# Performance work log

Measured on AMD Instinct MI355X. Metric: run time of the kernel, lower is better.

The kernel has to match this reference:

```python
import jax, jax.numpy as jnp
from jax import lax
import numpy as np

LOGZERO = -1e10  # matches the repo's `logzero` sentinel


def setup_inputs() -> dict:
    key = jax.random.key(0)
    k1, k2, k3, k4 = jax.random.split(key, 4)
    bs, xmax, vocab, ymax = 32, 1024, 1000, 128
    # CTC log-probabilities (ctc_generator output is log_softmax in the repo)
    ctc_out = jax.nn.log_softmax(
        jax.random.normal(k1, (bs, xmax, vocab), jnp.float32), axis=-1)
    src_size = jax.random.randint(k2, (bs,), xmax // 2, xmax + 1)
    src_mask = (jnp.arange(xmax)[None, :] < src_size[:, None])[:, None, :]  # [bs,1,xmax] bool
    ys = jax.random.randint(k3, (bs, ymax), 1, vocab)   # non-blank labels
    ylens = jax.random.randint(k4, (bs,), ymax // 2, ymax + 1)
    return {"ctc_out": ctc_out, "src_mask": src_mask, "src_size": src_size,
            "ys": ys, "ylens": ylens, "blank": 0}


def reference(ctc_out, src_mask, src_size, ys, ylens, blank):
    bs, xmax, vocab = ctc_out.shape
    ymax = ys.shape[1]
    L = 2 * ymax + 1  # blank-interleaved path length

    # mask invalid frames to logzero (masked_fill in torch)
    lp = jnp.where(src_mask.transpose(0, 2, 1), ctc_out, LOGZERO)  # [bs,xmax,vocab]

    # blank-interleaved path: [blank, y1, blank, y2, ..., blank]
    path = jnp.full((bs, L), blank, dtype=ys.dtype).at[:, 1::2].set(ys)
    path_lens = 2 * ylens + 1

    # log-probs gathered along the path: [xmax, bs, L] (time-major for scan)
    lp_path = jnp.take_along_axis(
        lp, jnp.broadcast_to(path[:, None, :], (bs, xmax, L)), axis=2)
    lp_path = lp_path.transpose(1, 0, 2)

    same_tr = path[:, :-2] == path[:, 2:]                 # [bs, L-2]
    idx = jnp.arange(L)
    outside = idx[None, :] >= path_lens[:, None]          # [bs, L]

    alpha0 = jnp.full((bs, L), LOGZERO, jnp.float32).at[:, 0].set(0.0)

    def step(alpha, lp_t):
        m0 = alpha
        m1 = jnp.concatenate([jnp.full((bs, 1), LOGZERO, alpha.dtype), alpha[:, :-1]], axis=1)
        m2 = jnp.concatenate([jnp.full((bs, 2), LOGZERO, alpha.dtype),
                              jnp.where(same_tr, LOGZERO, alpha[:, :-2])], axis=1)
        mat = jnp.stack([m0, m1, m2])                     # [3, bs, L]
        max_prob = jnp.max(mat, axis=0)
        arg = jnp.argmax(mat, axis=0)
        bp_t = idx[None, :] - arg                          # back-pointer (path position)
        max_prob = jnp.where(outside, LOGZERO, max_prob)
        alpha_new = max_prob + lp_t
        return alpha_new, (alpha_new, bp_t)

    _, (alpha_hist, bp) = lax.scan(step, alpha0, lp_path)  # [xmax,bs,L] each
    alpha_full = jnp.concatenate([alpha0[None], alpha_hist], axis=0)  # [xmax+1,bs,L]

    b_idx = jnp.arange(bs)
    alpha_at = alpha_full[src_size, b_idx]                 # [bs, L] alpha at t = src_size
    s1 = alpha_at[b_idx, path_lens - 1]
    s2 = alpha_at[b_idx, path_lens - 2]
    start = jnp.where(s1 > s2, path_lens - 1, path_lens - 2)
    score = jnp.maximum(s1, s2)                            # best alignment log-prob per utt

    # vectorized backtrace over all batches (reverse scan over time)
    def back_step(carry, t):
        tt = jnp.minimum(t + 1, xmax - 1)
        prev = bp[tt, b_idx, carry]                        # bp[b, t+1, state_{t+1}]
        val = jnp.where(t == src_size - 1, start,
                        jnp.where(t < src_size - 1, prev, 0))
        return val, val

    ts = jnp.arange(xmax - 1, -1, -1)
    _, states_rev = lax.scan(back_step, jnp.zeros((bs,), start.dtype), ts)
    states = states_rev[::-1].T                            # [bs, xmax] path positions

    aligned = jnp.take_along_axis(path, states, axis=1)    # [bs, xmax] tokens
    shift = jnp.concatenate([jnp.zeros((bs, 1), aligned.dtype), aligned[:, :-1]], axis=1)
    aligned = jnp.where(aligned == shift, 0, aligned)      # collapse repeats to 0
    shift2 = jnp.concatenate([jnp.zeros((bs, 1), aligned.dtype), aligned[:, :-1]], axis=1)

    csum = jnp.cumsum((shift2 != blank).astype(jnp.int32), axis=1)  # [bs, xmax]
    tm = csum[:, None, :] == jnp.arange(ymax + 1)[None, :, None]    # [bs, ymax+1, xmax]
    last = tm[:, -1, :] & src_mask[:, 0, :]
    last = last.at[b_idx, src_size - 1].set(True)
    tm = tm.at[:, -1, :].set(last)
    trigger_mask = tm & src_mask                           # & x_mask from FaNat.forward

    return score, trigger_mask, ylens + 1
```

## Files before the change

### kernel.cpp

```cpp
#include <hip/hip_runtime.h>
#include <stdint.h>

#define LOGZERO (-1e10f)

static constexpr int BS    = 32;
static constexpr int XMAX  = 1024;
static constexpr int VOCAB = 1000;
static constexpr int YMAX  = 128;
static constexpr int NROWS = YMAX + 1;
static constexpr int CH    = 8;
static constexpr int NPROD = 8;
static constexpr int NWAVES = 1 + NPROD;
static constexpr int NPAIR = XMAX / 2;

__global__ __launch_bounds__(64 * NWAVES) void k_viterbi(
    const float* __restrict__ ctc, const int* __restrict__ src_size,
    const int* __restrict__ ys, const int* __restrict__ ylens,
    const int* __restrict__ blankp, int* __restrict__ csum_ws,
    float* __restrict__ out)
{
    __shared__ float buf[2][CH][256];
    __shared__ unsigned char  bpb[XMAX * 64];
    __shared__ unsigned char  bp256[XMAX];
    __shared__ unsigned short bp2[NPAIR * 64];
    __shared__ unsigned char  bp2_256[NPAIR];
    __shared__ unsigned short st_lds[XMAX];
    __shared__ int ysl[YMAX];

    const int b    = blockIdx.x;
    const int tid  = threadIdx.x;
    const int wid  = tid >> 6;
    const int lane = tid & 63;
    const int ss   = src_size[b];
    const int yl   = ylens[b];
    const int bv   = blankp[0];
    const int plen = 2 * yl + 1;
    const float LZ = LOGZERO;

    for (int j = tid; j < YMAX; j += 64 * NWAVES) ysl[j] = ys[b * YMAX + j];
    for (int t = tid; t < XMAX; t += 64 * NWAVES) st_lds[t] = 0;
    __syncthreads();

    const int nchunk = (ss + CH - 1) / CH;
    const float* baseg = ctc + (size_t)b * XMAX * VOCAB;

    int start = 0;

    if (wid == 0) {
        const bool al1 = (lane > 0) && (ysl[2 * lane] != ysl[2 * lane - 1]);
        const bool al3 = (ysl[2 * lane + 1] != ysl[2 * lane]);
        const bool o0 = (4 * lane     >= plen);
        const bool o1 = (4 * lane + 1 >= plen);
        const bool o2 = (4 * lane + 2 >= plen);
        const bool o3 = (4 * lane + 3 >= plen);
        const bool o4 = (256 >= plen);
        const int rotidx = (lane + 63) & 63;

        float a0 = (lane == 0) ? 0.0f : LZ;
        float a1 = LZ, a2 = LZ, a3 = LZ, a4 = LZ;

        for (int c = 0; c < nchunk; ++c) {
            __syncthreads();
            const int cb = c & 1;
            float4 q[CH];
            #pragma unroll
            for (int r = 0; r < CH; ++r)
                q[r] = *reinterpret_cast<const float4*>(&buf[cb][r][lane * 4]);
            #pragma unroll
            for (int r = 0; r < CH; ++r) {
                const int t = c * CH + r;
                if (t < ss) {
                    float rot = __shfl(a3, rotidx);
                    float p3 = (lane == 0) ? LZ : rot;
                    float m0 = a0; int g0 = 0; if (p3 > m0) { m0 = p3; g0 = 1; }
                    float m1 = a1; int g1 = 0; if (a0 > m1) { m1 = a0; g1 = 1; }
                    float sk1 = al1 ? p3 : LZ;  if (sk1 > m1) { m1 = sk1; g1 = 2; }
                    float m2 = a2; int g2 = 0; if (a1 > m2) { m2 = a1; g2 = 1; }
                    float m3 = a3; int g3 = 0; if (a2 > m3) { m3 = a2; g3 = 1; }
                    float sk3 = al3 ? a1 : LZ;  if (sk3 > m3) { m3 = sk3; g3 = 2; }
                    float m4 = a4; int g4 = 0; if (rot > m4) { m4 = rot; g4 = 1; }
                    a0 = (o0 ? LZ : m0) + q[r].x;
                    a1 = (o1 ? LZ : m1) + q[r].y;
                    a2 = (o2 ? LZ : m2) + q[r].z;
                    a3 = (o3 ? LZ : m3) + q[r].w;
                    a4 = (o4 ? LZ : m4) + q[r].x;
                    bpb[t * 64 + lane] =
                        (unsigned char)(g0 | (g1 << 2) | (g2 << 4) | (g3 << 6));
                    if (lane == 0) bp256[t] = (unsigned char)g4;
                }
            }
        }

        auto getA = [&](int idx) -> float {
            if (idx == 256) return __shfl(a4, 0);
            int k = idx & 3;
            float pick = (k == 0) ? a0 : (k == 1) ? a1 : (k == 2) ? a2 : a3;
            return __shfl(pick, idx >> 2);
        };
        const float s1v = getA(plen - 1), s2v = getA(plen - 2);
        const float score = (s1v > s2v) ? s1v : s2v;
        start = (s1v > s2v) ? (plen - 1) : (plen - 2);
        if (lane == 0) {
            out[b] = score;
            out[32 + (size_t)BS * NROWS * XMAX + b] = (float)(yl + 1);
        }
    } else {
        const int pr = wid - 1;
        const int tokA = ysl[2 * lane];
        const int tokB = ysl[2 * lane + 1];
        int t0 = pr; if (t0 >= ss) t0 = ss - 1;
        const float* r0 = baseg + (size_t)t0 * VOCAB;
        float vb = r0[bv], va = r0[tokA], vc = r0[tokB];
        for (int c = 0; c < nchunk; ++c) {
            *reinterpret_cast<float4*>(&buf[c & 1][pr][lane * 4]) =
                make_float4(vb, va, vb, vc);
            int tn = (c + 1) * CH + pr; if (tn >= ss) tn = ss - 1;
            const float* r = baseg + (size_t)tn * VOCAB;
            vb = r[bv]; va = r[tokA]; vc = r[tokB];
            __syncthreads();
        }
    }
    __syncthreads();

    const int pmax = (ss - 1) >> 1;
    for (int p = 1 + wid; p <= pmax; p += NWAVES) {
        int oOdd  = bpb[(2 * p + 1) * 64 + lane];
        int oEven = bpb[(2 * p) * 64 + lane];
        int uEven = (lane > 0) ? bpb[(2 * p) * 64 + lane - 1] : 0;
        int evenWin = uEven | (oEven << 8);
        unsigned int acc = 0;
        #pragma unroll
        for (int k = 0; k < 4; ++k) {
            int a1v = (oOdd >> (2 * k)) & 3;
            int sh  = 2 * k - 2 * a1v + 8;
            int a2v = (evenWin >> sh) & 3;
            acc |= (unsigned)(a1v | (a2v << 2)) << (4 * k);
        }
        bp2[p * 64 + lane] = (unsigned short)acc;
        int a16 = bp256[2 * p + 1];
        int a26 = (a16 == 0) ? bp256[2 * p] : ((bpb[(2 * p) * 64 + 63] >> 6) & 3);
        if (lane == 0) bp2_256[p] = (unsigned char)(a16 | (a26 << 2));
    }
    __syncthreads();

    if (tid == 0) {
        int s = start, tc = ss - 1;
        st_lds[tc] = (unsigned short)s;
        if ((tc & 1) == 0 && tc >= 1) {
            int arg;
            if (s == 256) arg = bp256[tc];
            else arg = (bpb[tc * 64 + (s >> 2)] >> ((s & 3) * 2)) & 3;
            s -= arg; --tc; st_lds[tc] = (unsigned short)s;
        }
        while (tc > 1) {
            int n;
            if (s == 256) n = bp2_256[tc >> 1];
            else n = (bp2[(tc >> 1) * 64 + (s >> 2)] >> ((s & 3) * 4)) & 0xF;
            int sA = s - (n & 3);
            int sB = sA - (n >> 2);
            st_lds[tc - 1] = (unsigned short)sA;
            st_lds[tc - 2] = (unsigned short)sB;
            s = sB; tc -= 2;
        }
        if (tc == 1) {
            int arg;
            if (s == 256) arg = bp256[1];
            else arg = (bpb[64 + (s >> 2)] >> ((s & 3) * 2)) & 3;
            s -= arg; st_lds[0] = (unsigned short)s;
        }
    }
    __syncthreads();

    if (wid == 0) {
        auto tok_lds = [&](int stv) -> int { return (stv & 1) ? ysl[stv >> 1] : bv; };
        const int t0c = lane * 16;
        int prev_raw = (t0c == 0) ? 0 : tok_lds(st_lds[t0c - 1]);
        int cnt = 0;
        int csl[16];
        #pragma unroll
        for (int i = 0; i < 16; ++i) {
            int raw = tok_lds(st_lds[t0c + i]);
            int ac = (raw == prev_raw) ? 0 : raw;
            prev_raw = raw;
            csl[i] = cnt;
            cnt += (ac != bv) ? 1 : 0;
        }
        int v = cnt;
        #pragma unroll
        for (int off = 1; off < 64; off <<= 1) {
            int u = __shfl_up(v, off);
            if (lane >= off) v += u;
        }
        const int base_c = v - cnt;
        int* co = csum_ws + b * XMAX + t0c;
        #pragma unroll
        for (int i = 0; i < 16; ++i) co[i] = base_c + csl[i];
    }
}

__global__ __launch_bounds__(256) void k_mask(
    const int* __restrict__ csum_ws, const int* __restrict__ src_size,
    float* __restrict__ out)
{
    int bj = blockIdx.x;
    int b = bj / NROWS, j = bj - b * NROWS;
    int ss = src_size[b];
    const int* cs = csum_ws + b * XMAX;
    float* orow = out + 32 + (size_t)bj * XMAX;
    int t = threadIdx.x * 4;
    float4 v;
    float* vp = &v.x;
    #pragma unroll
    for (int i = 0; i < 4; ++i) {
        int tt = t + i;
        int c = cs[tt];
        bool in = tt < ss;
        bool val;
        if (j < YMAX) val = (c == j) && in;
        else          val = ((c == YMAX) || (tt == ss - 1)) && in;
        vp[i] = val ? 1.0f : 0.0f;
    }
    *(float4*)(orow + t) = v;
}

extern "C" void kernel_launch(void* const* d_in, const int* in_sizes, int n_in,
                              void* d_out, int out_size, void* d_ws, size_t ws_size,
                              hipStream_t stream) {
    const float* ctc      = (const float*)d_in[0];
    const int*   src_size = (const int*)d_in[2];
    const int*   ys       = (const int*)d_in[3];
    const int*   ylens    = (const int*)d_in[4];
    const int*   blankp   = (const int*)d_in[5];
    float* out = (float*)d_out;
    int*   csum_ws = (int*)d_ws;

    k_viterbi<<<BS, 64 * NWAVES, 0, stream>>>(ctc, src_size, ys, ylens, blankp,
                                              csum_ws, out);
    k_mask<<<BS * NROWS, 256, 0, stream>>>(csum_ws, src_size, out);
}
```

Measured before the change: 354.3 us.

## Pre-gather path log-probs into a compact workspace with a wide parallel kernel

Adds a k_gather kernel that uses many blocks to gather each frame's label and blank log-probs into a compact 132-float row in workspace. The Viterbi producer waves then read contiguous float2 values from that buffer instead of doing scattered loads from the full vocab rows. The intent is to take the latency-bound scattered gather off the serial 32-block Viterbi kernel and spread it across the whole GPU. The cost is an extra launch and a round-trip through workspace, and the new path only runs when the workspace is large enough.

```diff
diff --git a/kernel.cpp b/kernel.cpp
--- a/kernel.cpp
+++ b/kernel.cpp
@@ -8,16 +8,36 @@
 static constexpr int VOCAB = 1000;
 static constexpr int YMAX  = 128;
 static constexpr int NROWS = YMAX + 1;
+static constexpr int LPROW = 132;
 static constexpr int CH    = 8;
 static constexpr int NPROD = 8;
 static constexpr int NWAVES = 1 + NPROD;
 static constexpr int NPAIR = XMAX / 2;
 
+__global__ __launch_bounds__(256) void k_gather(
+    const float* __restrict__ ctc, const int* __restrict__ src_size,
+    const int* __restrict__ ys, const int* __restrict__ blankp,
+    float* __restrict__ lp)
+{
+    const int b    = blockIdx.x >> 8;
+    const int t    = ((blockIdx.x & 255) << 2) + (threadIdx.x >> 6);
+    const int lane = threadIdx.x & 63;
+    if (t >= src_size[b]) return;
+    const float* row = ctc + ((size_t)b * XMAX + t) * VOCAB;
+    float* orow      = lp  + ((size_t)b * XMAX + t) * LPROW;
+    const int tok0 = ys[b * YMAX + lane];
+    const int tok1 = ys[b * YMAX + 64 + lane];
+    orow[lane]      = row[tok0];
+    orow[64 + lane] = row[tok1];
+    if (lane == 0) orow[128] = row[blankp[0]];
+}
+
+template<int STAGED>
 __global__ __launch_bounds__(64 * NWAVES) void k_viterbi(
-    const float* __restrict__ ctc, const int* __restrict__ src_size,
-    const int* __restrict__ ys, const int* __restrict__ ylens,
-    const int* __restrict__ blankp, int* __restrict__ csum_ws,
-    float* __restrict__ out)
+    const float* __restrict__ ctc, const float* __restrict__ lp,
+    const int* __restrict__ src_size, const int* __restrict__ ys,
+    const int* __restrict__ ylens, const int* __restrict__ blankp,
+    int* __restrict__ csum_ws, float* __restrict__ out)
 {
     __shared__ float buf[2][CH][256];
     __shared__ unsigned char  bpb[XMAX * 64];
@@ -43,6 +63,7 @@
 
     const int nchunk = (ss + CH - 1) / CH;
     const float* baseg = ctc + (size_t)b * XMAX * VOCAB;
+    const float* basel = lp  + (size_t)b * XMAX * LPROW;
 
     int start = 0;
 
@@ -106,18 +127,34 @@
         }
     } else {
         const int pr = wid - 1;
-        const int tokA = ysl[2 * lane];
-        const int tokB = ysl[2 * lane + 1];
-        int t0 = pr; if (t0 >= ss) t0 = ss - 1;
-        const float* r0 = baseg + (size_t)t0 * VOCAB;
-        float vb = r0[bv], va = r0[tokA], vc = r0[tokB];
-        for (int c = 0; c < nchunk; ++c) {
-            *reinterpret_cast<float4*>(&buf[c & 1][pr][lane * 4]) =
-                make_float4(vb, va, vb, vc);
-            int tn = (c + 1) * CH + pr; if (tn >= ss) tn = ss - 1;
-            const float* r = baseg + (size_t)tn * VOCAB;
-            vb = r[bv]; va = r[tokA]; vc = r[tokB];
-            __syncthreads();
+        if (STAGED) {
+            int t0 = pr; if (t0 >= ss) t0 = ss - 1;
+            const float* r0 = basel + (size_t)t0 * LPROW;
+            float2 v = *reinterpret_cast<const float2*>(r0 + 2 * lane);
+            float vb = r0[128];
+            for (int c = 0; c < nchunk; ++c) {
+                *reinterpret_cast<float4*>(&buf[c & 1][pr][lane * 4]) =
+                    make_float4(vb, v.x, vb, v.y);
+                int tn = (c + 1) * CH + pr; if (tn >= ss) tn = ss - 1;
+                const float* r = basel + (size_t)tn * LPROW;
+                v = *reinterpret_cast<const float2*>(r + 2 * lane);
+                vb = r[128];
+                __syncthreads();
+            }
+        } else {
+            const int tokA = ysl[2 * lane];
+            const int tokB = ysl[2 * lane + 1];
+            int t0 = pr; if (t0 >= ss) t0 = ss - 1;
+            const float* r0 = baseg + (size_t)t0 * VOCAB;
+            float vb = r0[bv], va = r0[tokA], vc = r0[tokB];
+            for (int c = 0; c < nchunk; ++c) {
+                *reinterpret_cast<float4*>(&buf[c & 1][pr][lane * 4]) =
+                    make_float4(vb, va, vb, vc);
+                int tn = (c + 1) * CH + pr; if (tn >= ss) tn = ss - 1;
+                const float* r = baseg + (size_t)tn * VOCAB;
+                vb = r[bv]; va = r[tokA]; vc = r[tokB];
+                __syncthreads();
+            }
         }
     }
     __syncthreads();
@@ -232,9 +269,20 @@
     const int*   ylens    = (const int*)d_in[4];
     const int*   blankp   = (const int*)d_in[5];
     float* out = (float*)d_out;
-    int*   csum_ws = (int*)d_ws;
-
-    k_viterbi<<<BS, 64 * NWAVES, 0, stream>>>(ctc, src_size, ys, ylens, blankp,
-                                              csum_ws, out);
+
+    size_t lp_bytes = (size_t)BS * XMAX * LPROW * sizeof(float);
+    size_t cs_bytes = (size_t)BS * XMAX * sizeof(int);
+    int staged = (ws_size >= lp_bytes + cs_bytes) ? 1 : 0;
+    float* lp_path = (float*)d_ws;
+    int*   csum_ws = staged ? (int*)((char*)d_ws + lp_bytes) : (int*)d_ws;
+
+    if (staged) {
+        k_gather<<<BS * 256, 256, 0, stream>>>(ctc, src_size, ys, blankp, lp_path);
+        k_viterbi<1><<<BS, 64 * NWAVES, 0, stream>>>(ctc, lp_path, src_size, ys,
+                                                     ylens, blankp, csum_ws, out);
+    } else {
+        k_viterbi<0><<<BS, 64 * NWAVES, 0, stream>>>(ctc, lp_path, src_size, ys,
+                                                     ylens, blankp, csum_ws, out);
+    }
     k_mask<<<BS * NROWS, 256, 0, stream>>>(csum_ws, src_size, out);
 }
```

Result: slower. 394.4 us (+11.3%).

## Pre-gather path log-probs in separate kernel and use atomic producer-consumer ring

Applied to the files above, without the earlier changes.

Adds a fully parallel gather kernel that pulls the blank and label log-probs for every frame into a compact 132-float-per-row workspace. The Viterbi kernel then reads these compact rows with vector loads instead of making scattered gathers from the full vocab rows. Block-wide __syncthreads handoff between producer and consumer waves is replaced by LDS atomic counters over a 2-slot ring with 16-frame chunks. The pair backpointers are now packed in place in bpb, dropping the bp2 array, with a saved side copy for the odd tail. The cost is an extra kernel launch and a global round trip through the workspace, plus spin-wait risk on the counters.

```diff
diff --git a/kernel.cpp b/kernel.cpp
--- a/kernel.cpp
+++ b/kernel.cpp
@@ -8,24 +8,45 @@
 static constexpr int VOCAB = 1000;
 static constexpr int YMAX  = 128;
 static constexpr int NROWS = YMAX + 1;
-static constexpr int CH    = 8;
+static constexpr int LPROW = 132;
+static constexpr int CH    = 16;
+static constexpr int RING  = 2;
 static constexpr int NPROD = 8;
 static constexpr int NWAVES = 1 + NPROD;
 static constexpr int NPAIR = XMAX / 2;
 
+__global__ __launch_bounds__(256) void k_gather(
+    const float* __restrict__ ctc, const int* __restrict__ src_size,
+    const int* __restrict__ ys, const int* __restrict__ blankp,
+    float* __restrict__ lp)
+{
+    const int b    = blockIdx.x >> 8;
+    const int t    = ((blockIdx.x & 255) << 2) + (threadIdx.x >> 6);
+    const int lane = threadIdx.x & 63;
+    if (t >= src_size[b]) return;
+    const float* row = ctc + ((size_t)b * XMAX + t) * VOCAB;
+    float* orow      = lp  + ((size_t)b * XMAX + t) * LPROW;
+    const int tok0 = ys[b * YMAX + lane];
+    const int tok1 = ys[b * YMAX + 64 + lane];
+    orow[lane]      = row[tok0];
+    orow[64 + lane] = row[tok1];
+    if (lane == 0) orow[128] = row[blankp[0]];
+}
+
 __global__ __launch_bounds__(64 * NWAVES) void k_viterbi(
-    const float* __restrict__ ctc, const int* __restrict__ src_size,
+    const float* __restrict__ lp, const int* __restrict__ src_size,
     const int* __restrict__ ys, const int* __restrict__ ylens,
     const int* __restrict__ blankp, int* __restrict__ csum_ws,
     float* __restrict__ out)
 {
-    __shared__ float buf[2][CH][256];
+    __shared__ float buf[RING][CH][256];
     __shared__ unsigned char  bpb[XMAX * 64];
     __shared__ unsigned char  bp256[XMAX];
-    __shared__ unsigned short bp2[NPAIR * 64];
     __shared__ unsigned char  bp2_256[NPAIR];
     __shared__ unsigned short st_lds[XMAX];
+    __shared__ unsigned char  side_raw[64];
     __shared__ int ysl[YMAX];
+    __shared__ int prod_cnt, cons_cnt;
 
     const int b    = blockIdx.x;
     const int tid  = threadIdx.x;
@@ -39,10 +60,11 @@
 
     for (int j = tid; j < YMAX; j += 64 * NWAVES) ysl[j] = ys[b * YMAX + j];
     for (int t = tid; t < XMAX; t += 64 * NWAVES) st_lds[t] = 0;
+    if (tid == 0) { prod_cnt = 0; cons_cnt = 0; }
     __syncthreads();
 
     const int nchunk = (ss + CH - 1) / CH;
-    const float* baseg = ctc + (size_t)b * XMAX * VOCAB;
+    const float* basel = lp + (size_t)b * XMAX * LPROW;
 
     int start = 0;
 
@@ -60,12 +82,16 @@
         float a1 = LZ, a2 = LZ, a3 = LZ, a4 = LZ;
 
         for (int c = 0; c < nchunk; ++c) {
-            __syncthreads();
-            const int cb = c & 1;
+            while (__hip_atomic_load(&prod_cnt, __ATOMIC_ACQUIRE,
+                                     __HIP_MEMORY_SCOPE_WORKGROUP) < NPROD * (c + 1)) {}
+            const int slot = c & (RING - 1);
             float4 q[CH];
             #pragma unroll
             for (int r = 0; r < CH; ++r)
-                q[r] = *reinterpret_cast<const float4*>(&buf[cb][r][lane * 4]);
+                q[r] = *reinterpret_cast<const float4*>(&buf[slot][r][lane * 4]);
+            if (lane == 0)
+                __hip_atomic_fetch_add(&cons_cnt, 1, __ATOMIC_RELEASE,
+                                       __HIP_MEMORY_SCOPE_WORKGROUP);
             #pragma unroll
             for (int r = 0; r < CH; ++r) {
                 const int t = c * CH + r;
@@ -105,21 +131,42 @@
             out[32 + (size_t)BS * NROWS * XMAX + b] = (float)(yl + 1);
         }
     } else {
-        const int pr = wid - 1;
-        const int tokA = ysl[2 * lane];
-        const int tokB = ysl[2 * lane + 1];
-        int t0 = pr; if (t0 >= ss) t0 = ss - 1;
-        const float* r0 = baseg + (size_t)t0 * VOCAB;
-        float vb = r0[bv], va = r0[tokA], vc = r0[tokB];
+        const int r0 = wid - 1;
+        int t0 = r0;              if (t0 >= ss) t0 = ss - 1;
+        int t1 = r0 + NPROD;      if (t1 >= ss) t1 = ss - 1;
+        const float* p0 = basel + (size_t)t0 * LPROW;
+        const float* p1 = basel + (size_t)t1 * LPROW;
+        float2 vA0 = *reinterpret_cast<const float2*>(p0 + 2 * lane);
+        float  vb0 = p0[128];
+        float2 vA1 = *reinterpret_cast<const float2*>(p1 + 2 * lane);
+        float  vb1 = p1[128];
         for (int c = 0; c < nchunk; ++c) {
-            *reinterpret_cast<float4*>(&buf[c & 1][pr][lane * 4]) =
-                make_float4(vb, va, vb, vc);
-            int tn = (c + 1) * CH + pr; if (tn >= ss) tn = ss - 1;
-            const float* r = baseg + (size_t)tn * VOCAB;
-            vb = r[bv]; va = r[tokA]; vc = r[tokB];
-            __syncthreads();
-        }
-    }
+            if (c >= RING) {
+                while (__hip_atomic_load(&cons_cnt, __ATOMIC_ACQUIRE,
+                                         __HIP_MEMORY_SCOPE_WORKGROUP) < c - RING + 1)
+                    __builtin_amdgcn_s_sleep(1);
+            }
+            const int slot = c & (RING - 1);
+            *reinterpret_cast<float4*>(&buf[slot][r0][lane * 4]) =
+                make_float4(vb0, vA0.x, vb0, vA0.y);
+            *reinterpret_cast<float4*>(&buf[slot][r0 + NPROD][lane * 4]) =
+                make_float4(vb1, vA1.x, vb1, vA1.y);
+            if (lane == 0)
+                __hip_atomic_fetch_add(&prod_cnt, 1, __ATOMIC_RELEASE,
+                                       __HIP_MEMORY_SCOPE_WORKGROUP);
+            int tn0 = (c + 1) * CH + r0;         if (tn0 >= ss) tn0 = ss - 1;
+            int tn1 = (c + 1) * CH + r0 + NPROD; if (tn1 >= ss) tn1 = ss - 1;
+            const float* q0 = basel + (size_t)tn0 * LPROW;
+            const float* q1 = basel + (size_t)tn1 * LPROW;
+            vA0 = *reinterpret_cast<const float2*>(q0 + 2 * lane);
+            vb0 = q0[128];
+            vA1 = *reinterpret_cast<const float2*>(q1 + 2 * lane);
+            vb1 = q1[128];
+        }
+    }
+    __syncthreads();
+
+    if (wid == 0 && (((ss - 1) & 1) == 0)) side_raw[lane] = bpb[(ss - 1) * 64 + lane];
     __syncthreads();
 
     const int pmax = (ss - 1) >> 1;
@@ -127,18 +174,20 @@
         int oOdd  = bpb[(2 * p + 1) * 64 + lane];
         int oEven = bpb[(2 * p) * 64 + lane];
         int uEven = (lane > 0) ? bpb[(2 * p) * 64 + lane - 1] : 0;
+        int a26raw = (__shfl(oEven, 63) >> 6) & 3;
         int evenWin = uEven | (oEven << 8);
-        unsigned int acc = 0;
+        int nib[4];
         #pragma unroll
         for (int k = 0; k < 4; ++k) {
             int a1v = (oOdd >> (2 * k)) & 3;
             int sh  = 2 * k - 2 * a1v + 8;
             int a2v = (evenWin >> sh) & 3;
-            acc |= (unsigned)(a1v | (a2v << 2)) << (4 * k);
-        }
-        bp2[p * 64 + lane] = (unsigned short)acc;
+            nib[k] = a1v | (a2v << 2);
+        }
+        bpb[(2 * p) * 64 + lane]     = (unsigned char)(nib[0] | (nib[1] << 4));
+        bpb[(2 * p + 1) * 64 + lane] = (unsigned char)(nib[2] | (nib[3] << 4));
         int a16 = bp256[2 * p + 1];
-        int a26 = (a16 == 0) ? bp256[2 * p] : ((bpb[(2 * p) * 64 + 63] >> 6) & 3);
+        int a26 = (a16 == 0) ? bp256[2 * p] : a26raw;
         if (lane == 0) bp2_256[p] = (unsigned char)(a16 | (a26 << 2));
     }
     __syncthreads();
@@ -146,26 +195,28 @@
     if (tid == 0) {
         int s = start, tc = ss - 1;
         st_lds[tc] = (unsigned short)s;
-        if ((tc & 1) == 0 && tc >= 1) {
-            int arg;
-            if (s == 256) arg = bp256[tc];
-            else arg = (bpb[tc * 64 + (s >> 2)] >> ((s & 3) * 2)) & 3;
+        if ((tc & 1) == 0) {
+            int arg = (s == 256) ? bp256[tc]
+                                 : ((side_raw[s >> 2] >> ((s & 3) * 2)) & 3);
             s -= arg; --tc; st_lds[tc] = (unsigned short)s;
         }
-        while (tc > 1) {
-            int n;
-            if (s == 256) n = bp2_256[tc >> 1];
-            else n = (bp2[(tc >> 1) * 64 + (s >> 2)] >> ((s & 3) * 4)) & 0xF;
-            int sA = s - (n & 3);
-            int sB = sA - (n >> 2);
+        while (tc >= 3) {
+            int sA, sB;
+            if (s == 256) {
+                int n = bp2_256[tc >> 1];
+                sA = s - (n & 3); sB = sA - ((n >> 2) & 3);
+            } else {
+                int byv = bpb[(((tc >> 1) * 2) + ((s >> 1) & 1)) * 64 + (s >> 2)];
+                int n = (byv >> (4 * (s & 1))) & 0xF;
+                sA = s - (n & 3); sB = sA - ((n >> 2) & 3);
+            }
             st_lds[tc - 1] = (unsigned short)sA;
             st_lds[tc - 2] = (unsigned short)sB;
             s = sB; tc -= 2;
         }
         if (tc == 1) {
-            int arg;
-            if (s == 256) arg = bp256[1];
-            else arg = (bpb[64 + (s >> 2)] >> ((s & 3) * 2)) & 3;
+            int arg = (s == 256) ? bp256[1]
+                                 : ((bpb[64 + (s >> 2)] >> ((s & 3) * 2)) & 3);
             s -= arg; st_lds[0] = (unsigned short)s;
         }
     }
@@ -232,9 +283,13 @@
     const int*   ylens    = (const int*)d_in[4];
     const int*   blankp   = (const int*)d_in[5];
     float* out = (float*)d_out;
-    int*   csum_ws = (int*)d_ws;
-
-    k_viterbi<<<BS, 64 * NWAVES, 0, stream>>>(ctc, src_size, ys, ylens, blankp,
-                                              csum_ws, out);
+
+    size_t lp_bytes = (size_t)BS * XMAX * LPROW * sizeof(float);
+    float* lp_path = (float*)d_ws;
+    int*   csum_ws = (int*)((char*)d_ws + lp_bytes);
+
+    k_gather<<<BS * 256, 256, 0, stream>>>(ctc, src_size, ys, blankp, lp_path);
+    k_viterbi<<<BS, 64 * NWAVES, 0, stream>>>(lp_path, src_size, ys, ylens,
+                                              blankp, csum_ws, out);
     k_mask<<<BS * NROWS, 256, 0, stream>>>(csum_ws, src_size, out);
 }
```

Result: slower. 394.5 us (+11.3%).
